# Performance work log

Measured on AMD Instinct MI355X. Metric: run time of the kernel, lower is better.

The kernel has to match this reference:

```python
import math
import jax, jax.numpy as jnp
import numpy as np

D = 4096      # model dim
H = 32        # query heads
KVH = 8       # kv heads (GQA)
HD = D // H   # head dim = 128
B = 8         # batch == max_batch_size (cache returns full batch)
MAXLEN = 2048 # max_seq_len (cache length)
SEQ = 16      # new tokens this step
START = 1024  # start_pos (cache fill level)


def setup_inputs() -> dict:
    key = jax.random.key(0)
    ks = jax.random.split(key, 8)
    s = 0.02  # weight init scale
    x = jax.random.normal(ks[0], (B, SEQ, D), jnp.float32)
    wq = jax.random.normal(ks[1], (D, H * HD), jnp.float32) * s
    wk = jax.random.normal(ks[2], (D, KVH * HD), jnp.float32) * s
    wv = jax.random.normal(ks[3], (D, KVH * HD), jnp.float32) * s
    wo = jax.random.normal(ks[4], (H * HD, D), jnp.float32) * s
    # rotary tables: freqs_cis = exp(i * t * theta_j) -> (cos, sin)
    inv_freq = 1.0 / (10000.0 ** (jnp.arange(0, HD, 2, dtype=jnp.float32) / HD))  # [HD//2]
    ang = jnp.arange(MAXLEN, dtype=jnp.float32)[:, None] * inv_freq[None, :]      # [MAXLEN, HD//2]
    cos, sin = jnp.cos(ang), jnp.sin(ang)
    cache_k = jax.random.normal(ks[5], (B, MAXLEN, KVH, HD), jnp.float32)
    cache_v = jax.random.normal(ks[6], (B, MAXLEN, KVH, HD), jnp.float32)
    return dict(x=x, wq=wq, wk=wk, wv=wv, wo=wo, cos=cos, sin=sin,
                cache_k=cache_k, cache_v=cache_v, start_pos=START)


def _rotary(t, cos, sin):
    # t: [B,S,h,HD] viewed as complex pairs on last dim; cos/sin: [S, HD//2]
    tr = t.reshape(*t.shape[:-1], HD // 2, 2)
    t0, t1 = tr[..., 0], tr[..., 1]
    c = cos[None, :, None, :]
    s = sin[None, :, None, :]
    o0 = t0 * c - t1 * s
    o1 = t0 * s + t1 * c
    return jnp.stack([o0, o1], axis=-1).reshape(t.shape)


def reference(x, wq, wk, wv, wo, cos, sin, cache_k, cache_v, start_pos):
    bsz, seqlen, _ = x.shape
    q = (x @ wq).reshape(bsz, seqlen, H, HD)
    k = (x @ wk).reshape(bsz, seqlen, KVH, HD)
    v = (x @ wv).reshape(bsz, seqlen, KVH, HD)
    # rotary embedding on the current positions (fp32 like the original)
    cs = jax.lax.dynamic_slice_in_dim(cos, start_pos, seqlen, 0)
    sn = jax.lax.dynamic_slice_in_dim(sin, start_pos, seqlen, 0)
    q = _rotary(q.astype(jnp.float32), cs, sn).astype(x.dtype)
    k = _rotary(k.astype(jnp.float32), cs, sn).astype(x.dtype)
    # KV-cache update; attention runs over the full cache length
    keys = jax.lax.dynamic_update_slice(cache_k, k, (0, start_pos, 0, 0))
    vals = jax.lax.dynamic_update_slice(cache_v, v, (0, start_pos, 0, 0))
    # GQA repeat (tile-per-kv-head == jnp.repeat on head axis)
    n_rep = H // KVH
    keys = jnp.repeat(keys, n_rep, axis=2)  # [B, MAXLEN, H, HD]
    vals = jnp.repeat(vals, n_rep, axis=2)
    scores = jnp.einsum('bqhd,bkhd->bhqk', q, keys) / math.sqrt(HD)
    # pad mask from cache fill level (combine_masks with mask=None)
    valid = jnp.arange(keys.shape[1]) < start_pos + seqlen  # [MAXLEN]
    neg = jnp.asarray(-jnp.inf, scores.dtype)
    scores = jnp.where(valid[None, None, None, :], scores, neg)
    probs = jax.nn.softmax(scores.astype(jnp.float32), axis=-1).astype(q.dtype)
    out = jnp.einsum('bhqk,bkhd->bqhd', probs, vals).reshape(bsz, seqlen, H * HD)
    return out @ wo
```

## Files before the change

kernel.cpp:

```cpp
#include <hip/hip_runtime.h>
#include <math.h>
#include <stdint.h>

#define D 4096
#define H 32
#define KVH 8
#define HD 128
#define B_ 8
#define SEQ 16
#define MAXLEN 2048
#define NTOK 128
#define KSPLIT 8
#define KCH 512
#define BK 32
#define TSTEPS (KCH / BK)
#define KSA 16

typedef __attribute__((ext_vector_type(8))) short bh8;
typedef __attribute__((ext_vector_type(4))) float f32x4;
typedef _Float16 f16x2 __attribute__((ext_vector_type(2)));
typedef _Float16 f16x8 __attribute__((ext_vector_type(8)));

static __device__ __forceinline__ int imin(int a, int b) { return a < b ? a : b; }

static __device__ __forceinline__ short f2bf(float x) {
    union { float f; uint32_t u; } v; v.f = x;
    uint32_t u = v.u;
    return (short)((u + 0x7fffu + ((u >> 16) & 1u)) >> 16);
}
static __device__ __forceinline__ float bf2f(short b) {
    union { uint32_t u; float f; } v; v.u = ((uint32_t)(uint16_t)b) << 16;
    return v.f;
}

static __device__ __forceinline__ float fexp2(float x) {
#if __has_builtin(__builtin_amdgcn_exp2f)
    return __builtin_amdgcn_exp2f(x);
#else
    return exp2f(x);
#endif
}

__global__ __launch_bounds__(256) void cvt_x(const float* __restrict__ x, short* __restrict__ xp) {
    int i = blockIdx.x * 256 + threadIdx.x;
    int row = i >> 10;
    int c4 = (i & 1023) << 2;
    const float4 v = ((const float4*)x)[i];
    short4 o;
    o.x = f2bf(v.x); o.y = f2bf(v.y); o.z = f2bf(v.z); o.w = f2bf(v.w);
    *(short4*)&xp[((size_t)((c4 >> 3) * 128 + row)) * 8 + (c4 & 7)] = o;
}

__global__ __launch_bounds__(256) void gemm_mfma(const short* __restrict__ xp,
                                                 const float* __restrict__ wq,
                                                 const float* __restrict__ wk,
                                                 const float* __restrict__ wv,
                                                 short* __restrict__ Pq,
                                                 short* __restrict__ Pk,
                                                 short* __restrict__ Pv) {
    const int cbid = blockIdx.x;
    const int ks = blockIdx.y;
    const float* W; short* P; int ntot; int cb;
    if (cbid < 64)      { W = wq; P = Pq; ntot = 4096; cb = cbid * 64; }
    else if (cbid < 80) { W = wk; P = Pk; ntot = 1024; cb = (cbid - 64) * 64; }
    else                { W = wv; P = Pv; ntot = 1024; cb = (cbid - 80) * 64; }
    const int tid = threadIdx.x;
    const int lane = tid & 63;
    const int w = tid >> 6;
    const int wm = w >> 1, wn = w & 1;
    const int lrow = lane & 15, lkg = lane >> 4;
    const int k0 = ks * KCH;

    f32x4 acc[4][2];
#pragma unroll
    for (int fm = 0; fm < 4; ++fm)
#pragma unroll
        for (int fn = 0; fn < 2; ++fn) acc[fm][fn] = (f32x4){0.f, 0.f, 0.f, 0.f};

    const short* abase = xp + ((size_t)((k0 >> 3) + lkg) * 128 + wm * 64 + lrow) * 8;
    const float* wbase = W + (size_t)(k0 + lkg * 8) * ntot + cb + wn * 32 + lrow;

    auto loadWf = [&](int t, float (&wr)[16]) {
        const float* p = wbase + (size_t)t * 32 * ntot;
#pragma unroll
        for (int j = 0; j < 8; ++j) {
            wr[j]     = p[0];
            wr[8 + j] = p[16];
            p += ntot;
        }
    };
    auto loadAf = [&](int t, bh8 (&ar)[4]) {
        const short* p = abase + (size_t)t * 4096;
#pragma unroll
        for (int fm = 0; fm < 4; ++fm)
            ar[fm] = *(const bh8*)(p + fm * 128);
    };
    auto comp = [&](const bh8 (&ar)[4], const float (&wr)[16]) {
        bh8 bf0, bf1;
#pragma unroll
        for (int j = 0; j < 8; ++j) { bf0[j] = f2bf(wr[j]); bf1[j] = f2bf(wr[8 + j]); }
#pragma unroll
        for (int fm = 0; fm < 4; ++fm) {
            acc[fm][0] = __builtin_amdgcn_mfma_f32_16x16x32_bf16(ar[fm], bf0, acc[fm][0], 0, 0, 0);
            acc[fm][1] = __builtin_amdgcn_mfma_f32_16x16x32_bf16(ar[fm], bf1, acc[fm][1], 0, 0, 0);
        }
    };

    float wr0[16], wr1[16];
    bh8 ar0[4], ar1[4];
    loadWf(0, wr0); loadAf(0, ar0);
    for (int t = 0; t < TSTEPS; t += 2) {
        loadWf(t + 1, wr1); loadAf(t + 1, ar1);
        comp(ar0, wr0);
        if (t + 2 < TSTEPS) { loadWf(t + 2, wr0); loadAf(t + 2, ar0); }
        comp(ar1, wr1);
    }

    short* pp = P + (size_t)ks * NTOK * ntot;
#pragma unroll
    for (int fm = 0; fm < 4; ++fm) {
        const int gr0 = wm * 64 + fm * 16 + lkg * 4;
#pragma unroll
        for (int fn = 0; fn < 2; ++fn) {
            const int gc = cb + wn * 32 + fn * 16 + lrow;
#pragma unroll
            for (int q = 0; q < 4; ++q)
                pp[(size_t)(gr0 + q) * ntot + gc] = f2bf(acc[fm][fn][q]);
        }
    }
}

__global__ __launch_bounds__(256) void combine_rot(const short* __restrict__ Pq,
                                                   const short* __restrict__ Pk,
                                                   const short* __restrict__ Pv,
                                                   float* __restrict__ qb,
                                                   float* __restrict__ knb,
                                                   float* __restrict__ vnb,
                                                   const float* __restrict__ cosT,
                                                   const float* __restrict__ sinT,
                                                   const int* __restrict__ startp) {
    int gid = blockIdx.x * 256 + threadIdx.x;
    int tok = gid / 3072;
    int pr = gid % 3072;
    int col = pr * 2;
    int start = *startp;
    int pos = start + (tok & (SEQ - 1));
    float a = 0.f, b = 0.f;
    if (col < 4096) {
        const short* base = Pq + (size_t)tok * 4096 + col;
#pragma unroll
        for (int ks = 0; ks < KSPLIT; ++ks) {
            short2 t = *(const short2*)(base + (size_t)ks * NTOK * 4096);
            a += bf2f(t.x); b += bf2f(t.y);
        }
        int i = (col & 127) >> 1;
        float c = cosT[pos * 64 + i], s = sinT[pos * 64 + i];
        qb[(size_t)tok * 4096 + col]     = a * c - b * s;
        qb[(size_t)tok * 4096 + col + 1] = a * s + b * c;
    } else if (col < 5120) {
        int colr = col - 4096;
        const short* base = Pk + (size_t)tok * 1024 + colr;
#pragma unroll
        for (int ks = 0; ks < KSPLIT; ++ks) {
            short2 t = *(const short2*)(base + (size_t)ks * NTOK * 1024);
            a += bf2f(t.x); b += bf2f(t.y);
        }
        int i = (colr & 127) >> 1;
        float c = cosT[pos * 64 + i], s = sinT[pos * 64 + i];
        knb[(size_t)tok * 1024 + colr]     = a * c - b * s;
        knb[(size_t)tok * 1024 + colr + 1] = a * s + b * c;
    } else {
        int colr = col - 5120;
        const short* base = Pv + (size_t)tok * 1024 + colr;
#pragma unroll
        for (int ks = 0; ks < KSPLIT; ++ks) {
            short2 t = *(const short2*)(base + (size_t)ks * NTOK * 1024);
            a += bf2f(t.x); b += bf2f(t.y);
        }
        vnb[(size_t)tok * 1024 + colr]     = a;
        vnb[(size_t)tok * 1024 + colr + 1] = b;
    }
}

__global__ __launch_bounds__(256) void attn_fused(const float* __restrict__ qb,
                                                  const float* __restrict__ knb,
                                                  const float* __restrict__ vnb,
                                                  const float* __restrict__ ck,
                                                  const float* __restrict__ cv,
                                                  short* __restrict__ Opart,
                                                  float* __restrict__ mpart,
                                                  float* __restrict__ lpart,
                                                  const int* __restrict__ startp) {
    const int ksb = blockIdx.x;
    const int kvh = blockIdx.y;
    const int b   = blockIdx.z;
    const int start = *startp;
    const int klen = start + SEQ;
    const int chunk = (klen + KSA - 1) / KSA;
    const int bbeg = ksb * chunk;
    const int bend = imin(bbeg + chunk, klen);
    const int tiles = (chunk + 31) >> 5;

    const int tid = threadIdx.x;
    const int w = tid >> 6, lane = tid & 63;
    const int c = lane & 15, g = lane >> 4;
    const int hh = kvh * 4 + w;

    __shared__ __align__(16) _Float16 Ksh[2][16][32][8];
    __shared__ __align__(16) _Float16 Vsh[2][4][128][8];

    const float scl2 = 0.08838834764831843f * 1.4426950408889634f;

    f16x8 qfr[4];
    {
        const float* qp = qb + (size_t)(b * SEQ + c) * 4096 + hh * 128 + 8 * g;
#pragma unroll
        for (int h = 0; h < 4; ++h) {
            float4 a = *(const float4*)(qp + 32 * h);
            float4 b2 = *(const float4*)(qp + 32 * h + 4);
            qfr[h][0] = (_Float16)(a.x * scl2);  qfr[h][1] = (_Float16)(a.y * scl2);
            qfr[h][2] = (_Float16)(a.z * scl2);  qfr[h][3] = (_Float16)(a.w * scl2);
            qfr[h][4] = (_Float16)(b2.x * scl2); qfr[h][5] = (_Float16)(b2.y * scl2);
            qfr[h][6] = (_Float16)(b2.z * scl2); qfr[h][7] = (_Float16)(b2.w * scl2);
        }
    }

    f32x4 acc_o[8];
#pragma unroll
    for (int dm = 0; dm < 8; ++dm) acc_o[dm] = (f32x4){0.f, 0.f, 0.f, 0.f};
    float mrun = -INFINITY, lrun = 0.f;

    const int s_   = tid & 31;
    const int dgA  = tid >> 5;
    const int koffK = 8 * ((s_ >> 2) & 3) + 4 * (s_ >> 4) + (s_ & 3);
    const int kg0 = tid >> 6, d0 = (tid & 63) * 2;

    float4 kr0, kr1, kr2, kr3;
    float2 vrw[8];
    auto gloadRaw = [&](int t) {
        const int kp = bbeg + t * 32 + koffK;
        kr0 = (float4){0.f,0.f,0.f,0.f}; kr1 = kr0; kr2 = kr0; kr3 = kr0;
        if (kp < bend) {
            const float* kr = (kp < start)
                ? ck + ((size_t)((b * MAXLEN + kp) * KVH + kvh)) * HD
                : knb + (size_t)(b * SEQ + kp - start) * 1024 + kvh * HD;
            kr0 = *(const float4*)(kr + dgA * 8);
            kr1 = *(const float4*)(kr + dgA * 8 + 4);
            kr2 = *(const float4*)(kr + dgA * 8 + 64);
            kr3 = *(const float4*)(kr + dgA * 8 + 68);
        }
#pragma unroll
        for (int j = 0; j < 8; ++j) {
            const int kpv = bbeg + t * 32 + kg0 * 8 + j;
            vrw[j] = (float2){0.f, 0.f};
            if (kpv < bend) {
                const float* vrp = (kpv < start)
                    ? cv + ((size_t)((b * MAXLEN + kpv) * KVH + kvh)) * HD + d0
                    : vnb + (size_t)(b * SEQ + kpv - start) * 1024 + kvh * HD + d0;
                vrw[j] = *(const float2*)vrp;
            }
        }
    };
    auto cvtStore = [&](int bf) {
        f16x8 ka, kb;
        ka[0]=(_Float16)kr0.x; ka[1]=(_Float16)kr0.y; ka[2]=(_Float16)kr0.z; ka[3]=(_Float16)kr0.w;
        ka[4]=(_Float16)kr1.x; ka[5]=(_Float16)kr1.y; ka[6]=(_Float16)kr1.z; ka[7]=(_Float16)kr1.w;
        kb[0]=(_Float16)kr2.x; kb[1]=(_Float16)kr2.y; kb[2]=(_Float16)kr2.z; kb[3]=(_Float16)kr2.w;
        kb[4]=(_Float16)kr3.x; kb[5]=(_Float16)kr3.y; kb[6]=(_Float16)kr3.z; kb[7]=(_Float16)kr3.w;
        *(f16x8*)&Ksh[bf][dgA][s_][0] = ka;
        *(f16x8*)&Ksh[bf][dgA + 8][s_][0] = kb;
        f16x8 w0, w1;
#pragma unroll
        for (int j = 0; j < 8; ++j) { w0[j] = (_Float16)vrw[j].x; w1[j] = (_Float16)vrw[j].y; }
        *(f16x8*)&Vsh[bf][kg0][d0][0] = w0;
        *(f16x8*)&Vsh[bf][kg0][d0 + 1][0] = w1;
    };

    gloadRaw(0);
    cvtStore(0);
    __syncthreads();

    int buf = 0;
    for (int t = 0; t < tiles; ++t) {
        if (t + 1 < tiles) gloadRaw(t + 1);
        const int nk = imin(32, bend - (bbeg + t * 32));

        f32x4 acc_s[2];
        acc_s[0] = (f32x4){0.f, 0.f, 0.f, 0.f};
        acc_s[1] = (f32x4){0.f, 0.f, 0.f, 0.f};
#pragma unroll
        for (int h = 0; h < 4; ++h) {
#pragma unroll
            for (int m = 0; m < 2; ++m) {
                const f16x8 afr = *(const f16x8*)&Ksh[buf][h * 4 + g][m * 16 + c][0];
                acc_s[m] = __builtin_amdgcn_mfma_f32_16x16x32_f16(afr, qfr[h], acc_s[m], 0, 0, 0);
            }
        }
        float s8[8];
#pragma unroll
        for (int m = 0; m < 2; ++m)
#pragma unroll
            for (int q = 0; q < 4; ++q) s8[m * 4 + q] = acc_s[m][q];
        if (nk < 32) {
#pragma unroll
            for (int jj = 0; jj < 8; ++jj)
                if (8 * g + jj >= nk) s8[jj] = -1e30f;
        }
        float tmax = s8[0];
#pragma unroll
        for (int jj = 1; jj < 8; ++jj) tmax = fmaxf(tmax, s8[jj]);
        tmax = fmaxf(tmax, __shfl_xor(tmax, 16));
        tmax = fmaxf(tmax, __shfl_xor(tmax, 32));
        if (__any(tmax > mrun + 11.5f)) {
            const float mn = fmaxf(mrun, tmax);
            const float fac = fexp2(mrun - mn);
            lrun *= fac;
#pragma unroll
            for (int dm = 0; dm < 8; ++dm) {
                acc_o[dm][0] *= fac; acc_o[dm][1] *= fac;
                acc_o[dm][2] *= fac; acc_o[dm][3] *= fac;
            }
            mrun = mn;
        }
        float pe[8];
#pragma unroll
        for (int jj = 0; jj < 8; ++jj) pe[jj] = fexp2(s8[jj] - mrun);
#pragma unroll
        for (int jj = 0; jj < 8; ++jj) lrun += pe[jj];
        f16x8 bp;
#pragma unroll
        for (int jj = 0; jj < 8; ++jj) bp[jj] = (_Float16)pe[jj];

#pragma unroll
        for (int dm = 0; dm < 8; ++dm) {
            const f16x8 av = *(const f16x8*)&Vsh[buf][g][dm * 16 + c][0];
            acc_o[dm] = __builtin_amdgcn_mfma_f32_16x16x32_f16(av, bp, acc_o[dm], 0, 0, 0);
        }

        if (t + 1 < tiles) cvtStore(buf ^ 1);
        __syncthreads();
        buf ^= 1;
    }

    lrun += __shfl_xor(lrun, 16);
    lrun += __shfl_xor(lrun, 32);

    const int base = ((b * KVH + kvh) * KSA + ksb) * 64;
    const int row = w * 16 + c;
#pragma unroll
    for (int dm = 0; dm < 8; ++dm) {
        short4 o4;
        o4.x = f2bf(acc_o[dm][0]); o4.y = f2bf(acc_o[dm][1]);
        o4.z = f2bf(acc_o[dm][2]); o4.w = f2bf(acc_o[dm][3]);
        *(short4*)&Opart[(size_t)(base + row) * 128 + dm * 16 + g * 4] = o4;
    }
    if (g == 0) { mpart[base + row] = mrun; lpart[base + row] = lrun; }
}

__global__ __launch_bounds__(256) void attn_merge(const short* __restrict__ Opart,
                                                  const float* __restrict__ mpart,
                                                  const float* __restrict__ lpart,
                                                  short* __restrict__ aob) {
    const int bkvh = blockIdx.x;
    const int tid = threadIdx.x;
    __shared__ float sf[KSA][64];
    __shared__ float sinvL[64];
    if (tid < 64) {
        const int row = tid;
        float M = -INFINITY;
#pragma unroll
        for (int ks = 0; ks < KSA; ++ks)
            M = fmaxf(M, mpart[(size_t)(bkvh * KSA + ks) * 64 + row]);
        float L = 0.f;
#pragma unroll
        for (int ks = 0; ks < KSA; ++ks) {
            float f = exp2f(mpart[(size_t)(bkvh * KSA + ks) * 64 + row] - M);
            sf[ks][row] = f;
            L += f * lpart[(size_t)(bkvh * KSA + ks) * 64 + row];
        }
        sinvL[row] = 1.f / L;
    }
    __syncthreads();
    const int b = bkvh >> 3, kvh = bkvh & 7;
    for (int e = tid; e < 2048; e += 256) {
        const int row = e >> 5;
        const int d4 = (e & 31) << 2;
        float a0 = 0.f, a1 = 0.f, a2 = 0.f, a3 = 0.f;
#pragma unroll
        for (int ks = 0; ks < KSA; ++ks) {
            const short4 sp = *(const short4*)&Opart[((size_t)(bkvh * KSA + ks) * 64 + row) * 128 + d4];
            const float f = sf[ks][row];
            a0 = fmaf(f, bf2f(sp.x), a0);
            a1 = fmaf(f, bf2f(sp.y), a1);
            a2 = fmaf(f, bf2f(sp.z), a2);
            a3 = fmaf(f, bf2f(sp.w), a3);
        }
        const float iL = sinvL[row];
        a0 *= iL; a1 *= iL; a2 *= iL; a3 *= iL;
        const int hh = kvh * 4 + (row >> 4);
        const int tok = b * SEQ + (row & 15);
        const int col = hh * 128 + d4;
        short4 o;
        o.x = f2bf(a0); o.y = f2bf(a1); o.z = f2bf(a2); o.w = f2bf(a3);
        *(short4*)&aob[((size_t)(col >> 3) * 128 + tok) * 8 + (col & 7)] = o;
    }
}

__global__ __launch_bounds__(256) void sum_parts(const short* __restrict__ P,
                                                 float* __restrict__ out) {
    int i = blockIdx.x * 256 + threadIdx.x;
    float a0 = 0.f, a1 = 0.f, a2 = 0.f, a3 = 0.f;
#pragma unroll
    for (int ks = 0; ks < KSPLIT; ++ks) {
        const short4 t = ((const short4*)(P + (size_t)ks * NTOK * 4096))[i];
        a0 += bf2f(t.x); a1 += bf2f(t.y); a2 += bf2f(t.z); a3 += bf2f(t.w);
    }
    ((float4*)out)[i] = make_float4(a0, a1, a2, a3);
}

extern "C" void kernel_launch(void* const* d_in, const int* in_sizes, int n_in,
                              void* d_out, int out_size, void* d_ws, size_t ws_size,
                              hipStream_t stream) {
    const float* x  = (const float*)d_in[0];
    const float* wq = (const float*)d_in[1];
    const float* wk = (const float*)d_in[2];
    const float* wv = (const float*)d_in[3];
    const float* wo = (const float*)d_in[4];
    const float* cs = (const float*)d_in[5];
    const float* sn = (const float*)d_in[6];
    const float* ck = (const float*)d_in[7];
    const float* cv = (const float*)d_in[8];
    const int* startp = (const int*)d_in[9];

    short* Opart = (short*)d_ws;
    short* Pqb = Opart;
    short* Pkb = Pqb + (size_t)KSPLIT * NTOK * 4096;
    short* Pvb = Pkb + (size_t)KSPLIT * NTOK * 1024;
    float* qb   = (float*)(Opart + (size_t)64 * KSA * 64 * 128);
    float* knb  = qb + (size_t)NTOK * 4096;
    float* vnb  = knb + (size_t)NTOK * 1024;
    short* xpre = (short*)(vnb + (size_t)NTOK * 1024);
    short* aob  = xpre + (size_t)NTOK * 4096;
    float* mpart = (float*)(aob + (size_t)NTOK * 4096);
    float* lpart = mpart + (size_t)64 * KSA * 64;

    cvt_x<<<512, 256, 0, stream>>>(x, xpre);
    gemm_mfma<<<dim3(96, KSPLIT), 256, 0, stream>>>(xpre, wq, wk, wv, Pqb, Pkb, Pvb);
    combine_rot<<<1536, 256, 0, stream>>>(Pqb, Pkb, Pvb, qb, knb, vnb, cs, sn, startp);
    attn_fused<<<dim3(KSA, KVH, B_), 256, 0, stream>>>(qb, knb, vnb, ck, cv, Opart, mpart, lpart, startp);
    attn_merge<<<64, 256, 0, stream>>>(Opart, mpart, lpart, aob);
    gemm_mfma<<<dim3(64, KSPLIT), 256, 0, stream>>>(aob, wo, wo, wo, Pqb, Pqb, Pqb);
    sum_parts<<<512, 256, 0, stream>>>(Pqb, (float*)d_out);
}
```

Measured before the change: 106.1 us.

## Stage QKV weight tiles through LDS with vectorized coalesced loads

The QKV projection kernel previously had each lane load scalar fp32 weight elements down columns, strided by ntot, straight into registers. It now loads float4 row segments cooperatively, converts them to bf16, and writes them transposed into a double-buffered shared-memory tile. MFMA B fragments are then read from LDS as 8-wide vectors. This aims to make weight streaming, the dominant memory traffic, coalesced and vectorized, at the cost of LDS writes and a barrier per K step.

After: 104.1 us. No clear change (-1.8%).

```diff
diff --git a/kernel.cpp b/kernel.cpp
--- a/kernel.cpp
+++ b/kernel.cpp
@@ -71,6 +71,8 @@
     const int lrow = lane & 15, lkg = lane >> 4;
     const int k0 = ks * KCH;
 
+    __shared__ __align__(16) short Wl[2][64][32];
+
     f32x4 acc[4][2];
 #pragma unroll
     for (int fm = 0; fm < 4; ++fm)
@@ -78,42 +80,64 @@
         for (int fn = 0; fn < 2; ++fn) acc[fm][fn] = (f32x4){0.f, 0.f, 0.f, 0.f};
 
     const short* abase = xp + ((size_t)((k0 >> 3) + lkg) * 128 + wm * 64 + lrow) * 8;
-    const float* wbase = W + (size_t)(k0 + lkg * 8) * ntot + cb + wn * 32 + lrow;
-
-    auto loadWf = [&](int t, float (&wr)[16]) {
-        const float* p = wbase + (size_t)t * 32 * ntot;
-#pragma unroll
-        for (int j = 0; j < 8; ++j) {
-            wr[j]     = p[0];
-            wr[8 + j] = p[16];
-            p += ntot;
-        }
-    };
-    auto loadAf = [&](int t, bh8 (&ar)[4]) {
+    const int n4 = (tid & 15) * 4;
+    const int r2 = (tid >> 4) * 2;
+    const float* wbase = W + (size_t)(k0 + r2) * ntot + cb + n4;
+
+    auto issueA = [&](int t, bh8 (&ar)[4]) {
         const short* p = abase + (size_t)t * 4096;
 #pragma unroll
         for (int fm = 0; fm < 4; ++fm)
             ar[fm] = *(const bh8*)(p + fm * 128);
     };
-    auto comp = [&](const bh8 (&ar)[4], const float (&wr)[16]) {
-        bh8 bf0, bf1;
-#pragma unroll
-        for (int j = 0; j < 8; ++j) { bf0[j] = f2bf(wr[j]); bf1[j] = f2bf(wr[8 + j]); }
-#pragma unroll
-        for (int fm = 0; fm < 4; ++fm) {
-            acc[fm][0] = __builtin_amdgcn_mfma_f32_16x16x32_bf16(ar[fm], bf0, acc[fm][0], 0, 0, 0);
-            acc[fm][1] = __builtin_amdgcn_mfma_f32_16x16x32_bf16(ar[fm], bf1, acc[fm][1], 0, 0, 0);
-        }
-    };
-
-    float wr0[16], wr1[16];
-    bh8 ar0[4], ar1[4];
-    loadWf(0, wr0); loadAf(0, ar0);
-    for (int t = 0; t < TSTEPS; t += 2) {
-        loadWf(t + 1, wr1); loadAf(t + 1, ar1);
-        comp(ar0, wr0);
-        if (t + 2 < TSTEPS) { loadWf(t + 2, wr0); loadAf(t + 2, ar0); }
-        comp(ar1, wr1);
+    auto issueW = [&](int t, float4& fa, float4& fb) {
+        const float* p = wbase + (size_t)t * 32 * ntot;
+        fa = *(const float4*)p;
+        fb = *(const float4*)(p + ntot);
+    };
+    auto storeW = [&](int bufw, const float4& fa, const float4& fb) {
+        *(short2*)&Wl[bufw][n4 + 0][r2] = make_short2(f2bf(fa.x), f2bf(fb.x));
+        *(short2*)&Wl[bufw][n4 + 1][r2] = make_short2(f2bf(fa.y), f2bf(fb.y));
+        *(short2*)&Wl[bufw][n4 + 2][r2] = make_short2(f2bf(fa.z), f2bf(fb.z));
+        *(short2*)&Wl[bufw][n4 + 3][r2] = make_short2(f2bf(fa.w), f2bf(fb.w));
+    };
+    auto compute = [&](int bufc, const bh8 (&ar)[4]) {
+#pragma unroll
+        for (int fn = 0; fn < 2; ++fn) {
+            const bh8 bfr = *(const bh8*)&Wl[bufc][wn * 32 + fn * 16 + lrow][lkg * 8];
+#pragma unroll
+            for (int fm = 0; fm < 4; ++fm)
+                acc[fm][fn] = __builtin_amdgcn_mfma_f32_16x16x32_bf16(ar[fm], bfr, acc[fm][fn], 0, 0, 0);
+        }
+    };
+
+    bh8 arE[4], arO[4];
+    float4 wEa, wEb, wOa, wOb;
+
+    issueA(0, arE);
+    issueW(0, wEa, wEb);
+    issueW(1, wOa, wOb);
+    storeW(0, wEa, wEb);
+    asm volatile("s_waitcnt lgkmcnt(0)" ::: "memory");
+    __builtin_amdgcn_s_barrier();
+
+#pragma unroll
+    for (int t = 0; t < TSTEPS; ++t) {
+        if ((t & 1) == 0) {
+            if (t + 1 < TSTEPS) issueA(t + 1, arO);
+            if (t + 2 < TSTEPS) issueW(t + 2, wEa, wEb);
+            compute(0, arE);
+            if (t + 1 < TSTEPS) storeW(1, wOa, wOb);
+        } else {
+            if (t + 1 < TSTEPS) issueA(t + 1, arE);
+            if (t + 2 < TSTEPS) issueW(t + 2, wOa, wOb);
+            compute(1, arO);
+            if (t + 1 < TSTEPS) storeW(0, wEa, wEb);
+        }
+        if (t + 1 < TSTEPS) {
+            asm volatile("s_waitcnt lgkmcnt(0)" ::: "memory");
+            __builtin_amdgcn_s_barrier();
+        }
     }
 
     short* pp = P + (size_t)ks * NTOK * ntot;
```

## Stage weight tiles in LDS via async global_load_lds with wider GEMM blocks

Applied to the files above, without the earlier changes.

Replaces the projection GEMM with a 512-thread kernel that covers 256 output columns per block. fp32 weight rows are staged into double-buffered, XOR-swizzled LDS with 16-byte global_load_lds transfers, replacing per-lane strided scalar loads. K-split is doubled to 16 to keep enough blocks in flight. The goal is better coalesced, overlapped streaming of the large fp32 weights, at the cost of twice the partial-sum traffic that the combine and sum kernels must read, and of a reshuffled workspace in which Opart aliases the partials buffer.

After: 124.8 us. 1.18x slower.

```diff
diff --git a/kernel.cpp b/kernel.cpp
--- a/kernel.cpp
+++ b/kernel.cpp
@@ -10,10 +10,10 @@
 #define SEQ 16
 #define MAXLEN 2048
 #define NTOK 128
-#define KSPLIT 8
-#define KCH 512
-#define BK 32
-#define TSTEPS (KCH / BK)
+#define KSPLIT 16
+#define KCH 256
+#define BKW 32
+#define WSTEPS (KCH / BKW)
 #define KSA 16
 
 typedef __attribute__((ext_vector_type(8))) short bh8;
@@ -39,6 +39,11 @@
 #else
     return exp2f(x);
 #endif
+}
+
+static __device__ __forceinline__ void gll16(const void* g, void* l) {
+    __builtin_amdgcn_global_load_lds((const __attribute__((address_space(1))) uint32_t*)g,
+                                     (__attribute__((address_space(3))) uint32_t*)l, 16, 0, 0);
 }
 
 __global__ __launch_bounds__(256) void cvt_x(const float* __restrict__ x, short* __restrict__ xp) {
@@ -51,69 +56,74 @@
     *(short4*)&xp[((size_t)((c4 >> 3) * 128 + row)) * 8 + (c4 & 7)] = o;
 }
 
-__global__ __launch_bounds__(256) void gemm_mfma(const short* __restrict__ xp,
-                                                 const float* __restrict__ wq,
-                                                 const float* __restrict__ wk,
-                                                 const float* __restrict__ wv,
-                                                 short* __restrict__ Pq,
-                                                 short* __restrict__ Pk,
-                                                 short* __restrict__ Pv) {
+__global__ __launch_bounds__(512, 4) void gemm_wide(const short* __restrict__ xp,
+                                                    const float* __restrict__ wq,
+                                                    const float* __restrict__ wk,
+                                                    const float* __restrict__ wv,
+                                                    short* __restrict__ Pq,
+                                                    short* __restrict__ Pk,
+                                                    short* __restrict__ Pv) {
     const int cbid = blockIdx.x;
     const int ks = blockIdx.y;
     const float* W; short* P; int ntot; int cb;
-    if (cbid < 64)      { W = wq; P = Pq; ntot = 4096; cb = cbid * 64; }
-    else if (cbid < 80) { W = wk; P = Pk; ntot = 1024; cb = (cbid - 64) * 64; }
-    else                { W = wv; P = Pv; ntot = 1024; cb = (cbid - 80) * 64; }
+    if (cbid < 16)      { W = wq; P = Pq; ntot = 4096; cb = cbid * 256; }
+    else if (cbid < 20) { W = wk; P = Pk; ntot = 1024; cb = (cbid - 16) * 256; }
+    else                { W = wv; P = Pv; ntot = 1024; cb = (cbid - 20) * 256; }
     const int tid = threadIdx.x;
     const int lane = tid & 63;
-    const int w = tid >> 6;
-    const int wm = w >> 1, wn = w & 1;
+    const int wv_ = tid >> 6;
+    const int wm = wv_ >> 2, wn = wv_ & 3;
     const int lrow = lane & 15, lkg = lane >> 4;
     const int k0 = ks * KCH;
-
-    f32x4 acc[4][2];
+    const int kxor = (lkg & 1) << 4;
+
+    __shared__ __align__(16) float Wt[2][BKW][256];
+
+    f32x4 acc[4][4];
 #pragma unroll
     for (int fm = 0; fm < 4; ++fm)
 #pragma unroll
-        for (int fn = 0; fn < 2; ++fn) acc[fm][fn] = (f32x4){0.f, 0.f, 0.f, 0.f};
+        for (int fn = 0; fn < 4; ++fn) acc[fm][fn] = (f32x4){0.f, 0.f, 0.f, 0.f};
 
     const short* abase = xp + ((size_t)((k0 >> 3) + lkg) * 128 + wm * 64 + lrow) * 8;
-    const float* wbase = W + (size_t)(k0 + lkg * 8) * ntot + cb + wn * 32 + lrow;
-
-    auto loadWf = [&](int t, float (&wr)[16]) {
-        const float* p = wbase + (size_t)t * 32 * ntot;
-#pragma unroll
-        for (int j = 0; j < 8; ++j) {
-            wr[j]     = p[0];
-            wr[8 + j] = p[16];
-            p += ntot;
+
+    auto stage = [&](int t, int bufw) {
+        char* ldsb = (char*)&Wt[bufw][0][0];
+#pragma unroll
+        for (int r = 0; r < 4; ++r) {
+            const int row = r * 8 + wv_;
+            const int xr = (r & 1) << 2;
+            const float* src = W + (size_t)(k0 + t * BKW + row) * ntot + cb + ((lane ^ xr) << 2);
+            gll16(src, ldsb + r * 8192 + tid * 16);
         }
     };
-    auto loadAf = [&](int t, bh8 (&ar)[4]) {
-        const short* p = abase + (size_t)t * 4096;
-#pragma unroll
-        for (int fm = 0; fm < 4; ++fm)
-            ar[fm] = *(const bh8*)(p + fm * 128);
-    };
-    auto comp = [&](const bh8 (&ar)[4], const float (&wr)[16]) {
-        bh8 bf0, bf1;
-#pragma unroll
-        for (int j = 0; j < 8; ++j) { bf0[j] = f2bf(wr[j]); bf1[j] = f2bf(wr[8 + j]); }
-#pragma unroll
-        for (int fm = 0; fm < 4; ++fm) {
-            acc[fm][0] = __builtin_amdgcn_mfma_f32_16x16x32_bf16(ar[fm], bf0, acc[fm][0], 0, 0, 0);
-            acc[fm][1] = __builtin_amdgcn_mfma_f32_16x16x32_bf16(ar[fm], bf1, acc[fm][1], 0, 0, 0);
-        }
-    };
-
-    float wr0[16], wr1[16];
-    bh8 ar0[4], ar1[4];
-    loadWf(0, wr0); loadAf(0, ar0);
-    for (int t = 0; t < TSTEPS; t += 2) {
-        loadWf(t + 1, wr1); loadAf(t + 1, ar1);
-        comp(ar0, wr0);
-        if (t + 2 < TSTEPS) { loadWf(t + 2, wr0); loadAf(t + 2, ar0); }
-        comp(ar1, wr1);
+
+    stage(0, 0);
+    __syncthreads();
+
+    int buf = 0;
+    for (int t = 0; t < WSTEPS; ++t) {
+        bh8 arr[4];
+        {
+            const short* p = abase + (size_t)t * 4096;
+#pragma unroll
+            for (int fm = 0; fm < 4; ++fm)
+                arr[fm] = *(const bh8*)(p + fm * 128);
+        }
+        if (t + 1 < WSTEPS) stage(t + 1, buf ^ 1);
+#pragma unroll
+        for (int fn = 0; fn < 4; ++fn) {
+            const int col = wn * 64 + fn * 16 + lrow;
+            bh8 bfr;
+#pragma unroll
+            for (int j = 0; j < 8; ++j)
+                bfr[j] = f2bf(Wt[buf][lkg * 8 + j][col ^ kxor]);
+#pragma unroll
+            for (int fm = 0; fm < 4; ++fm)
+                acc[fm][fn] = __builtin_amdgcn_mfma_f32_16x16x32_bf16(arr[fm], bfr, acc[fm][fn], 0, 0, 0);
+        }
+        __syncthreads();
+        buf ^= 1;
     }
 
     short* pp = P + (size_t)ks * NTOK * ntot;
@@ -121,8 +131,8 @@
     for (int fm = 0; fm < 4; ++fm) {
         const int gr0 = wm * 64 + fm * 16 + lkg * 4;
 #pragma unroll
-        for (int fn = 0; fn < 2; ++fn) {
-            const int gc = cb + wn * 32 + fn * 16 + lrow;
+        for (int fn = 0; fn < 4; ++fn) {
+            const int gc = cb + wn * 64 + fn * 16 + lrow;
 #pragma unroll
             for (int q = 0; q < 4; ++q)
                 pp[(size_t)(gr0 + q) * ntot + gc] = f2bf(acc[fm][fn][q]);
@@ -432,11 +442,11 @@
     const float* cv = (const float*)d_in[8];
     const int* startp = (const int*)d_in[9];
 
-    short* Opart = (short*)d_ws;
-    short* Pqb = Opart;
+    short* Pqb = (short*)d_ws;
     short* Pkb = Pqb + (size_t)KSPLIT * NTOK * 4096;
     short* Pvb = Pkb + (size_t)KSPLIT * NTOK * 1024;
-    float* qb   = (float*)(Opart + (size_t)64 * KSA * 64 * 128);
+    short* Opart = Pqb;
+    float* qb   = (float*)(Pvb + (size_t)KSPLIT * NTOK * 1024);
     float* knb  = qb + (size_t)NTOK * 4096;
     float* vnb  = knb + (size_t)NTOK * 1024;
     short* xpre = (short*)(vnb + (size_t)NTOK * 1024);
@@ -445,10 +455,10 @@
     float* lpart = mpart + (size_t)64 * KSA * 64;
 
     cvt_x<<<512, 256, 0, stream>>>(x, xpre);
-    gemm_mfma<<<dim3(96, KSPLIT), 256, 0, stream>>>(xpre, wq, wk, wv, Pqb, Pkb, Pvb);
+    gemm_wide<<<dim3(24, KSPLIT), 512, 0, stream>>>(xpre, wq, wk, wv, Pqb, Pkb, Pvb);
     combine_rot<<<1536, 256, 0, stream>>>(Pqb, Pkb, Pvb, qb, knb, vnb, cs, sn, startp);
     attn_fused<<<dim3(KSA, KVH, B_), 256, 0, stream>>>(qb, knb, vnb, ck, cv, Opart, mpart, lpart, startp);
     attn_merge<<<64, 256, 0, stream>>>(Opart, mpart, lpart, aob);
-    gemm_mfma<<<dim3(64, KSPLIT), 256, 0, stream>>>(aob, wo, wo, wo, Pqb, Pqb, Pqb);
+    gemm_wide<<<dim3(16, KSPLIT), 512, 0, stream>>>(aob, wo, wo, wo, Pqb, Pqb, Pqb);
     sum_parts<<<512, 256, 0, stream>>>(Pqb, (float*)d_out);
 }
```
